# Optimization experiments

Hardware: AMD Instinct MI355X
Metric: run time of the kernel (lower is better)

The kernel has to match this reference:

```python
import jax, jax.numpy as jnp
import numpy as np

N_NODES = 100000
N_EDGES = 1600000
N_GRAPHS = 256
IN_F = 64   # global_features (GNN input dim)
OUT_F = 64  # node_features (GNN output dim)


def setup_inputs() -> dict:
    key = jax.random.key(0)
    ks = jax.random.split(key, 8)
    x = jax.random.normal(ks[0], (N_NODES, IN_F), dtype=jnp.float32)
    edge_index = jax.random.randint(ks[1], (2, N_EDGES), 0, N_NODES, dtype=jnp.int64)
    batch = jnp.sort(jax.random.randint(ks[2], (N_NODES,), 0, N_GRAPHS, dtype=jnp.int64))
    # GNNLayer linear: in=global_features, out=node_features
    W_gnn = jax.random.normal(ks[3], (IN_F, OUT_F), dtype=jnp.float32) / np.sqrt(IN_F)
    b_gnn = jnp.zeros((OUT_F,), dtype=jnp.float32)
    # global_attention: Linear(node_features, 1)
    W_att = jax.random.normal(ks[4], (OUT_F, 1), dtype=jnp.float32) / np.sqrt(OUT_F)
    b_att = jnp.zeros((1,), dtype=jnp.float32)
    return {"x": x, "edge_index": edge_index, "batch": batch,
            "W_gnn": W_gnn, "b_gnn": b_gnn, "W_att": W_att, "b_att": b_att}


def reference(x, edge_index, batch, W_gnn, b_gnn, W_att, b_att):
    src, dst = edge_index[0], edge_index[1]
    # --- GNN message passing layer: aggregate neighbor features, transform ---
    agg = jax.ops.segment_sum(x[src], dst, num_segments=N_NODES)  # [N, IN_F]
    h = jax.nn.relu((x + agg) @ W_gnn + b_gnn)                    # [N, OUT_F]
    # --- attention scores + scatter softmax over batch segments ---
    scores = (h @ W_att + b_att)[:, 0]                            # [N]
    seg_max = jax.ops.segment_max(scores, batch, num_segments=N_GRAPHS)
    e = jnp.exp(scores - seg_max[batch])
    denom = jax.ops.segment_sum(e, batch, num_segments=N_GRAPHS)
    w = e / denom[batch]                                          # [N]
    # --- weighted scatter-add pooling ---
    out = jax.ops.segment_sum(w[:, None] * h, batch, num_segments=N_GRAPHS)
    return out  # [N_GRAPHS, OUT_F]
```

## Files before the change

kernel.cpp:

```cpp
#include <hip/hip_runtime.h>

#define N_NODES  100000
#define N_EDGES  1600000
#define N_GRAPHS 256
#define F        64

#define CHUNK    8192
#define NCHUNK   196
#define GBN      128
#define NB2      782
#define EDGE_CAP 2560

#define CAST_ELEMS   (N_NODES * F / 4)
#define CAST_BLOCKS  ((CAST_ELEMS + 1023) / 1024)
#define CPF_BLOCKS   (NB2 + CAST_BLOCKS)

__device__ __forceinline__ unsigned short f2bf(float f) {
    unsigned int u = __float_as_uint(f);
    u += 0x7FFFu + ((u >> 16) & 1u);
    return (unsigned short)(u >> 16);
}

__global__ __launch_bounds__(1024) void prep_kernel(
        const int* __restrict__ src, const int* __restrict__ dst,
        unsigned int* __restrict__ pairs, int* __restrict__ cstartT) {
    __shared__ int hist[NB2];
    __shared__ int cur[NB2];
    __shared__ int wsum[16];
    __shared__ unsigned int stage[CHUNK];
    int tid  = threadIdx.x;
    int c    = blockIdx.x;
    int base = c * CHUNK;
    int m    = min(CHUNK, N_EDGES - base);
    int lane = tid & 63;
    int w    = tid >> 6;

    for (int k = tid; k < NB2; k += 1024) hist[k] = 0;
    __syncthreads();
    for (int e = tid; e < m; e += 1024)
        atomicAdd(&hist[dst[base + e] >> 7], 1);
    __syncthreads();

    int v = (tid < NB2) ? hist[tid] : 0;
    #pragma unroll
    for (int o = 1; o < 64; o <<= 1) {
        int u = __shfl_up(v, o, 64);
        if (lane >= o) v += u;
    }
    if (lane == 63) wsum[w] = v;
    __syncthreads();
    if (tid < 16) {
        int s = wsum[tid];
        #pragma unroll
        for (int o = 1; o < 16; o <<= 1) {
            int u = __shfl_up(s, o, 64);
            if (tid >= o) s += u;
        }
        wsum[tid] = s;
    }
    __syncthreads();
    if (w > 0) v += wsum[w - 1];

    if (tid < NB2) {
        int excl = v - hist[tid];
        cur[tid] = excl;
        cstartT[tid * NCHUNK + c] = base + excl;
    }
    if (tid == 0) cstartT[NB2 * NCHUNK + c] = base + m;
    __syncthreads();
    for (int e = tid; e < m; e += 1024) {
        int d = dst[base + e];
        int slot = atomicAdd(&cur[d >> 7], 1);
        stage[slot] = ((unsigned)(d & (GBN - 1)) << 17) | (unsigned)src[base + e];
    }
    __syncthreads();
    for (int e = tid; e < m; e += 1024)
        pairs[base + e] = stage[e];
}

__global__ __launch_bounds__(1024) void compact_cast_kernel(
        const unsigned int* __restrict__ pairs,
        const int* __restrict__ cstartT,
        int* __restrict__ eidx,
        int* __restrict__ nbeg,
        int* __restrict__ nend,
        const float* __restrict__ x,
        unsigned short* __restrict__ xh,
        float* __restrict__ out, float* __restrict__ denom) {
    int tid = threadIdx.x;
    int b   = blockIdx.x;

    if (b >= NB2) {
        int ci = b - NB2;
        if (ci == 0) {
            for (int i = tid; i < N_GRAPHS * F; i += 1024) out[i] = 0.f;
            if (tid < N_GRAPHS) denom[tid] = 0.f;
        }
        int i = ci * 1024 + tid;
        if (i < CAST_ELEMS) {
            float4 v = ((const float4*)x)[i];
            ushort4 o;
            o.x = f2bf(v.x); o.y = f2bf(v.y); o.z = f2bf(v.z); o.w = f2bf(v.w);
            ((ushort4*)xh)[i] = o;
        }
        return;
    }

    __shared__ int rstart[NCHUNK];
    __shared__ int roff[NCHUNK + 1];
    __shared__ int wsum[16];
    __shared__ unsigned int epairs[EDGE_CAP];
    __shared__ int ncnt[GBN];
    __shared__ int ncur[GBN];

    int wave  = tid >> 6;
    int lane  = tid & 63;
    int node0 = b * GBN;
    int nn    = min(GBN, N_NODES - node0);
    int gbase = b * EDGE_CAP;

    int myrc = 0;
    if (tid < NCHUNK) {
        int a = cstartT[b * NCHUNK + tid];
        int n = cstartT[(b + 1) * NCHUNK + tid];
        rstart[tid] = a;
        myrc = n - a;
    }
    __syncthreads();

    {
        int v = myrc;
        #pragma unroll
        for (int o = 1; o < 64; o <<= 1) {
            int u = __shfl_up(v, o, 64);
            if (lane >= o) v += u;
        }
        if (lane == 63) wsum[wave] = v;
        __syncthreads();
        if (tid < 16) {
            int s = wsum[tid];
            #pragma unroll
            for (int o = 1; o < 16; o <<= 1) {
                int u = __shfl_up(s, o, 64);
                if (tid >= o) s += u;
            }
            wsum[tid] = s;
        }
        __syncthreads();
        if (wave > 0) v += wsum[wave - 1];
        if (tid < NCHUNK) roff[tid] = v - myrc;
        if (tid == NCHUNK - 1) roff[NCHUNK] = v;
    }
    __syncthreads();
    int E = roff[NCHUNK];

    for (int e = tid; e < E; e += 1024) {
        int lo = 0, hi = NCHUNK - 1;
        while (lo < hi) {
            int mid = (lo + hi + 1) >> 1;
            if (roff[mid] <= e) lo = mid; else hi = mid - 1;
        }
        epairs[e] = pairs[rstart[lo] + (e - roff[lo])];
    }
    __syncthreads();

    if (tid < GBN) ncnt[tid] = 0;
    __syncthreads();
    for (int e = tid; e < E; e += 1024)
        atomicAdd(&ncnt[epairs[e] >> 17], 1);
    __syncthreads();
    {
        int mycnt = (tid < GBN) ? ncnt[tid] : 0;
        int v = mycnt;
        #pragma unroll
        for (int o = 1; o < 64; o <<= 1) {
            int u = __shfl_up(v, o, 64);
            if (lane >= o) v += u;
        }
        if (lane == 63) wsum[wave] = v;
        __syncthreads();
        if (tid < 2) {
            int s = wsum[tid];
            int u = __shfl_up(s, 1, 64);
            if (tid >= 1) s += u;
            wsum[tid] = s;
        }
        __syncthreads();
        if (wave == 1) v += wsum[0];
        if (tid < GBN) {
            int excl = v - mycnt;
            ncur[tid] = excl;
            if (tid < nn) {
                nbeg[node0 + tid] = gbase + excl;
                nend[node0 + tid] = gbase + excl + mycnt;
            }
        }
    }
    __syncthreads();
    for (int e = tid; e < E; e += 1024) {
        unsigned int p = epairs[e];
        int slot = atomicAdd(&ncur[p >> 17], 1);
        eidx[gbase + slot] = (int)(p & 0x1FFFFu);
    }
}

#define NODES_PER_WAVE 25
#define GT_NWAVES  (N_NODES / NODES_PER_WAVE)
#define GT_BLOCKS  (GT_NWAVES / 4)

__device__ __forceinline__ float bfl(unsigned int u) { return __uint_as_float(u << 16); }
__device__ __forceinline__ float bfh(unsigned int u) { return __uint_as_float(u & 0xFFFF0000u); }

__global__ __launch_bounds__(256) void gather_pool_kernel(
        const unsigned short* __restrict__ xh,
        const int*   __restrict__ nbeg,
        const int*   __restrict__ nend,
        const int*   __restrict__ eidx,
        const int*   __restrict__ batch,
        const float* __restrict__ Wg,
        const float* __restrict__ bg,
        const float* __restrict__ Wa,
        const float* __restrict__ ba,
        float*       __restrict__ out_acc,
        float*       __restrict__ denom) {
    int tid  = threadIdx.x;
    int lane = tid & 63;
    int grp  = lane >> 3;
    int c    = lane & 7;
    int waveId = blockIdx.x * 4 + (tid >> 6);

    int n0   = waveId * NODES_PER_WAVE;
    int nEnd = n0 + NODES_PER_WAVE;

    float wcol[F];
    #pragma unroll
    for (int k = 0; k < F; ++k) wcol[k] = Wg[k * F + lane];
    float bgl = bg[lane];
    float wal = Wa[lane];
    float ba0 = ba[0];

    const uint4* xh4 = (const uint4*)xh;

    int   cur_g = batch[n0];
    float accw  = 0.f;
    float denw  = 0.f;

    int pb = nbeg[n0];
    int pe = nend[n0];
    int sl_cur = (pb + lane < pe) ? eidx[pb + lane] : 0;

    for (int n = n0; n < nEnd; ++n) {
        int start = pb, end = pe;
        int sl    = sl_cur;
        if (n + 1 < nEnd) {
            pb = nbeg[n + 1];
            pe = nend[n + 1];
            sl_cur = (pb + lane < pe) ? eidx[pb + lane] : 0;
        }

        float a0=0.f,a1=0.f,a2=0.f,a3=0.f,a4=0.f,a5=0.f,a6=0.f,a7=0.f;
        {
            int jmax = end - start; if (jmax > 64) jmax = 64;
            for (int j = 0; j < jmax; j += 8) {
                int el = j + grp;
                int s  = __shfl(sl, el, 64);
                if (el < jmax) {
                    uint4 v = xh4[s * 8 + c];
                    a0 += bfl(v.x); a1 += bfh(v.x);
                    a2 += bfl(v.y); a3 += bfh(v.y);
                    a4 += bfl(v.z); a5 += bfh(v.z);
                    a6 += bfl(v.w); a7 += bfh(v.w);
                }
            }
        }
        for (int base = start + 64; base < end; base += 64) {
            int jmax = end - base; if (jmax > 64) jmax = 64;
            int sl2 = (base + lane < end) ? eidx[base + lane] : 0;
            for (int j = 0; j < jmax; j += 8) {
                int el = j + grp;
                int s  = __shfl(sl2, el, 64);
                if (el < jmax) {
                    uint4 v = xh4[s * 8 + c];
                    a0 += bfl(v.x); a1 += bfh(v.x);
                    a2 += bfl(v.y); a3 += bfh(v.y);
                    a4 += bfl(v.z); a5 += bfh(v.z);
                    a6 += bfl(v.w); a7 += bfh(v.w);
                }
            }
        }
        #pragma unroll
        for (int o = 8; o <= 32; o <<= 1) {
            a0 += __shfl_xor(a0, o, 64); a1 += __shfl_xor(a1, o, 64);
            a2 += __shfl_xor(a2, o, 64); a3 += __shfl_xor(a3, o, 64);
            a4 += __shfl_xor(a4, o, 64); a5 += __shfl_xor(a5, o, 64);
            a6 += __shfl_xor(a6, o, 64); a7 += __shfl_xor(a7, o, 64);
        }
        {
            uint4 v = xh4[n * 8 + c];
            a0 += bfl(v.x); a1 += bfh(v.x);
            a2 += bfl(v.y); a3 += bfh(v.y);
            a4 += bfl(v.z); a5 += bfh(v.z);
            a6 += bfl(v.w); a7 += bfh(v.w);
        }

        float re[8] = {a0,a1,a2,a3,a4,a5,a6,a7};
        float q0=0.f,q1=0.f,q2=0.f,q3=0.f,q4=0.f,q5=0.f,q6=0.f,q7=0.f;
        #pragma unroll
        for (int k = 0; k < F; k += 8) {
            int ln = k >> 3;
            q0 += __int_as_float(__builtin_amdgcn_readlane(__float_as_int(re[0]), ln)) * wcol[k + 0];
            q1 += __int_as_float(__builtin_amdgcn_readlane(__float_as_int(re[1]), ln)) * wcol[k + 1];
            q2 += __int_as_float(__builtin_amdgcn_readlane(__float_as_int(re[2]), ln)) * wcol[k + 2];
            q3 += __int_as_float(__builtin_amdgcn_readlane(__float_as_int(re[3]), ln)) * wcol[k + 3];
            q4 += __int_as_float(__builtin_amdgcn_readlane(__float_as_int(re[4]), ln)) * wcol[k + 4];
            q5 += __int_as_float(__builtin_amdgcn_readlane(__float_as_int(re[5]), ln)) * wcol[k + 5];
            q6 += __int_as_float(__builtin_amdgcn_readlane(__float_as_int(re[6]), ln)) * wcol[k + 6];
            q7 += __int_as_float(__builtin_amdgcn_readlane(__float_as_int(re[7]), ln)) * wcol[k + 7];
        }
        float hv = ((q0 + q1) + (q2 + q3)) + ((q4 + q5) + (q6 + q7)) + bgl;
        hv = hv > 0.f ? hv : 0.f;

        float p = hv * wal;
        #pragma unroll
        for (int o = 32; o > 0; o >>= 1)
            p += __shfl_down(p, o, 64);
        float s = __int_as_float(__builtin_amdgcn_readlane(__float_as_int(p), 0)) + ba0;
        float e = __expf(s);

        int g = batch[n];
        if (g != cur_g) {
            atomicAdd(&out_acc[cur_g * F + lane], accw);
            if (lane == 0) atomicAdd(&denom[cur_g], denw);
            accw = 0.f; denw = 0.f; cur_g = g;
        }
        accw += e * hv;
        denw += e;
    }
    atomicAdd(&out_acc[cur_g * F + lane], accw);
    if (lane == 0) atomicAdd(&denom[cur_g], denw);
}

__global__ __launch_bounds__(256) void finalize_kernel(
        float* __restrict__ out, const float* __restrict__ denom) {
    int i = blockIdx.x * 256 + threadIdx.x;
    if (i >= N_GRAPHS * F) return;
    float d = denom[i >> 6];
    out[i] = (d > 0.f) ? out[i] / d : 0.f;
}

extern "C" void kernel_launch(void* const* d_in, const int* in_sizes, int n_in,
                              void* d_out, int out_size, void* d_ws, size_t ws_size,
                              hipStream_t stream) {
    const float* x     = (const float*)d_in[0];
    const int*   ei    = (const int*)d_in[1];
    const int*   batch = (const int*)d_in[2];
    const float* Wg    = (const float*)d_in[3];
    const float* bg    = (const float*)d_in[4];
    const float* Wa    = (const float*)d_in[5];
    const float* ba    = (const float*)d_in[6];
    float* out = (float*)d_out;

    const int* src = ei;
    const int* dst = ei + N_EDGES;

    char* ws = (char*)d_ws;
    unsigned short* xh      = (unsigned short*)(ws);
    unsigned int*   pairs   = (unsigned int*)(ws + 12800000);
    int*            cstartT = (int*)(ws + 19200000);
    int*            eidx    = (int*)(ws + 19814144);
    int*            nbeg    = (int*)(ws + 27821824);
    int*            nend    = (int*)(ws + 28221824);
    float*          denom   = (float*)(ws + 28621824);

    prep_kernel        <<<NCHUNK, 1024, 0, stream>>>(src, dst, pairs, cstartT);
    compact_cast_kernel<<<CPF_BLOCKS, 1024, 0, stream>>>(
        pairs, cstartT, eidx, nbeg, nend, x, xh, out, denom);
    gather_pool_kernel <<<GT_BLOCKS, 256, 0, stream>>>(
        xh, nbeg, nend, eidx, batch, Wg, bg, Wa, ba, out, denom);
    finalize_kernel    <<<(N_GRAPHS * F + 255) / 256, 256, 0, stream>>>(out, denom);
}
```

Before: 183.7 us.

## Replace two-level bucketed CSR build with global atomic histogram and scatter

The chunked two-pass bucket sort (prep and compact) that built a per-node edge list is replaced by four simple kernels. They zero a per-node count, build a global atomic histogram over dst, give each wavefront a contiguous range through a global atomic allocator, and scatter src indices with per-node atomic cursors. This drops the shared-memory staging and binary searches, but it relies on heavy global atomics to random addresses, and the edge order and node ranges become nondeterministic and non-monotonic. It also adds kernel launches.

Result: slower. 366.6 us (+99.6%).

```diff
diff --git a/kernel.cpp b/kernel.cpp
--- a/kernel.cpp
+++ b/kernel.cpp
@@ -5,15 +5,8 @@
 #define N_GRAPHS 256
 #define F        64
 
-#define CHUNK    8192
-#define NCHUNK   196
-#define GBN      128
-#define NB2      782
-#define EDGE_CAP 2560
-
-#define CAST_ELEMS   (N_NODES * F / 4)
-#define CAST_BLOCKS  ((CAST_ELEMS + 1023) / 1024)
-#define CPF_BLOCKS   (NB2 + CAST_BLOCKS)
+#define CAST_ELEMS (N_NODES * F / 4)
+
 
 __device__ __forceinline__ unsigned short f2bf(float f) {
     unsigned int u = __float_as_uint(f);
@@ -21,186 +14,65 @@
     return (unsigned short)(u >> 16);
 }
 
-__global__ __launch_bounds__(1024) void prep_kernel(
-        const int* __restrict__ src, const int* __restrict__ dst,
-        unsigned int* __restrict__ pairs, int* __restrict__ cstartT) {
-    __shared__ int hist[NB2];
-    __shared__ int cur[NB2];
-    __shared__ int wsum[16];
-    __shared__ unsigned int stage[CHUNK];
-    int tid  = threadIdx.x;
-    int c    = blockIdx.x;
-    int base = c * CHUNK;
-    int m    = min(CHUNK, N_EDGES - base);
-    int lane = tid & 63;
-    int w    = tid >> 6;
-
-    for (int k = tid; k < NB2; k += 1024) hist[k] = 0;
-    __syncthreads();
-    for (int e = tid; e < m; e += 1024)
-        atomicAdd(&hist[dst[base + e] >> 7], 1);
-    __syncthreads();
-
-    int v = (tid < NB2) ? hist[tid] : 0;
+__global__ __launch_bounds__(256) void init_cast_kernel(
+        const float* __restrict__ x, unsigned short* __restrict__ xh,
+        int* __restrict__ cnt, float* __restrict__ out,
+        float* __restrict__ denom, unsigned int* __restrict__ allocp) {
+    int gtid   = blockIdx.x * 256 + threadIdx.x;
+    int stride = gridDim.x * 256;
+    for (int i = gtid; i < CAST_ELEMS; i += stride) {
+        float4 v = ((const float4*)x)[i];
+        ushort4 o;
+        o.x = f2bf(v.x); o.y = f2bf(v.y); o.z = f2bf(v.z); o.w = f2bf(v.w);
+        ((ushort4*)xh)[i] = o;
+    }
+    for (int i = gtid; i < N_NODES; i += stride) cnt[i] = 0;
+    if (gtid < N_GRAPHS * F) out[gtid] = 0.f;
+    if (gtid < N_GRAPHS) denom[gtid] = 0.f;
+    if (gtid == 0) *allocp = 0u;
+}
+
+__global__ __launch_bounds__(256) void hist_kernel(
+        const int* __restrict__ dst, int* __restrict__ cnt) {
+    int gtid   = blockIdx.x * 256 + threadIdx.x;
+    int stride = gridDim.x * 256;
+    for (int e = gtid; e < N_EDGES; e += stride)
+        atomicAdd(&cnt[dst[e]], 1);
+}
+
+__global__ __launch_bounds__(256) void alloc_kernel(
+        const int* __restrict__ cnt,
+        int* __restrict__ nbeg, int* __restrict__ nend, int* __restrict__ cur,
+        unsigned int* __restrict__ allocp) {
+    int i    = blockIdx.x * 256 + threadIdx.x;
+    int lane = threadIdx.x & 63;
+    int c = (i < N_NODES) ? cnt[i] : 0;
+    int v = c;
     #pragma unroll
     for (int o = 1; o < 64; o <<= 1) {
         int u = __shfl_up(v, o, 64);
         if (lane >= o) v += u;
     }
-    if (lane == 63) wsum[w] = v;
-    __syncthreads();
-    if (tid < 16) {
-        int s = wsum[tid];
-        #pragma unroll
-        for (int o = 1; o < 16; o <<= 1) {
-            int u = __shfl_up(s, o, 64);
-            if (tid >= o) s += u;
-        }
-        wsum[tid] = s;
-    }
-    __syncthreads();
-    if (w > 0) v += wsum[w - 1];
-
-    if (tid < NB2) {
-        int excl = v - hist[tid];
-        cur[tid] = excl;
-        cstartT[tid * NCHUNK + c] = base + excl;
-    }
-    if (tid == 0) cstartT[NB2 * NCHUNK + c] = base + m;
-    __syncthreads();
-    for (int e = tid; e < m; e += 1024) {
-        int d = dst[base + e];
-        int slot = atomicAdd(&cur[d >> 7], 1);
-        stage[slot] = ((unsigned)(d & (GBN - 1)) << 17) | (unsigned)src[base + e];
-    }
-    __syncthreads();
-    for (int e = tid; e < m; e += 1024)
-        pairs[base + e] = stage[e];
-}
-
-__global__ __launch_bounds__(1024) void compact_cast_kernel(
-        const unsigned int* __restrict__ pairs,
-        const int* __restrict__ cstartT,
-        int* __restrict__ eidx,
-        int* __restrict__ nbeg,
-        int* __restrict__ nend,
-        const float* __restrict__ x,
-        unsigned short* __restrict__ xh,
-        float* __restrict__ out, float* __restrict__ denom) {
-    int tid = threadIdx.x;
-    int b   = blockIdx.x;
-
-    if (b >= NB2) {
-        int ci = b - NB2;
-        if (ci == 0) {
-            for (int i = tid; i < N_GRAPHS * F; i += 1024) out[i] = 0.f;
-            if (tid < N_GRAPHS) denom[tid] = 0.f;
-        }
-        int i = ci * 1024 + tid;
-        if (i < CAST_ELEMS) {
-            float4 v = ((const float4*)x)[i];
-            ushort4 o;
-            o.x = f2bf(v.x); o.y = f2bf(v.y); o.z = f2bf(v.z); o.w = f2bf(v.w);
-            ((ushort4*)xh)[i] = o;
-        }
-        return;
-    }
-
-    __shared__ int rstart[NCHUNK];
-    __shared__ int roff[NCHUNK + 1];
-    __shared__ int wsum[16];
-    __shared__ unsigned int epairs[EDGE_CAP];
-    __shared__ int ncnt[GBN];
-    __shared__ int ncur[GBN];
-
-    int wave  = tid >> 6;
-    int lane  = tid & 63;
-    int node0 = b * GBN;
-    int nn    = min(GBN, N_NODES - node0);
-    int gbase = b * EDGE_CAP;
-
-    int myrc = 0;
-    if (tid < NCHUNK) {
-        int a = cstartT[b * NCHUNK + tid];
-        int n = cstartT[(b + 1) * NCHUNK + tid];
-        rstart[tid] = a;
-        myrc = n - a;
-    }
-    __syncthreads();
-
-    {
-        int v = myrc;
-        #pragma unroll
-        for (int o = 1; o < 64; o <<= 1) {
-            int u = __shfl_up(v, o, 64);
-            if (lane >= o) v += u;
-        }
-        if (lane == 63) wsum[wave] = v;
-        __syncthreads();
-        if (tid < 16) {
-            int s = wsum[tid];
-            #pragma unroll
-            for (int o = 1; o < 16; o <<= 1) {
-                int u = __shfl_up(s, o, 64);
-                if (tid >= o) s += u;
-            }
-            wsum[tid] = s;
-        }
-        __syncthreads();
-        if (wave > 0) v += wsum[wave - 1];
-        if (tid < NCHUNK) roff[tid] = v - myrc;
-        if (tid == NCHUNK - 1) roff[NCHUNK] = v;
-    }
-    __syncthreads();
-    int E = roff[NCHUNK];
-
-    for (int e = tid; e < E; e += 1024) {
-        int lo = 0, hi = NCHUNK - 1;
-        while (lo < hi) {
-            int mid = (lo + hi + 1) >> 1;
-            if (roff[mid] <= e) lo = mid; else hi = mid - 1;
-        }
-        epairs[e] = pairs[rstart[lo] + (e - roff[lo])];
-    }
-    __syncthreads();
-
-    if (tid < GBN) ncnt[tid] = 0;
-    __syncthreads();
-    for (int e = tid; e < E; e += 1024)
-        atomicAdd(&ncnt[epairs[e] >> 17], 1);
-    __syncthreads();
-    {
-        int mycnt = (tid < GBN) ? ncnt[tid] : 0;
-        int v = mycnt;
-        #pragma unroll
-        for (int o = 1; o < 64; o <<= 1) {
-            int u = __shfl_up(v, o, 64);
-            if (lane >= o) v += u;
-        }
-        if (lane == 63) wsum[wave] = v;
-        __syncthreads();
-        if (tid < 2) {
-            int s = wsum[tid];
-            int u = __shfl_up(s, 1, 64);
-            if (tid >= 1) s += u;
-            wsum[tid] = s;
-        }
-        __syncthreads();
-        if (wave == 1) v += wsum[0];
-        if (tid < GBN) {
-            int excl = v - mycnt;
-            ncur[tid] = excl;
-            if (tid < nn) {
-                nbeg[node0 + tid] = gbase + excl;
-                nend[node0 + tid] = gbase + excl + mycnt;
-            }
-        }
-    }
-    __syncthreads();
-    for (int e = tid; e < E; e += 1024) {
-        unsigned int p = epairs[e];
-        int slot = atomicAdd(&ncur[p >> 17], 1);
-        eidx[gbase + slot] = (int)(p & 0x1FFFFu);
+    int base = 0;
+    if (lane == 63) base = (int)atomicAdd(allocp, (unsigned int)v);
+    base = __shfl(base, 63, 64);
+    if (i < N_NODES) {
+        int b = base + v - c;
+        nbeg[i] = b;
+        nend[i] = b + c;
+        cur[i]  = b;
+    }
+}
+
+__global__ __launch_bounds__(256) void scatter_kernel(
+        const int* __restrict__ src, const int* __restrict__ dst,
+        int* __restrict__ cur, int* __restrict__ eidx) {
+    int gtid   = blockIdx.x * 256 + threadIdx.x;
+    int stride = gridDim.x * 256;
+    for (int e = gtid; e < N_EDGES; e += stride) {
+        int d = dst[e];
+        int slot = atomicAdd(&cur[d], 1);
+        eidx[slot] = src[e];
     }
 }
 
@@ -364,18 +236,20 @@
     const int* dst = ei + N_EDGES;
 
     char* ws = (char*)d_ws;
-    unsigned short* xh      = (unsigned short*)(ws);
-    unsigned int*   pairs   = (unsigned int*)(ws + 12800000);
-    int*            cstartT = (int*)(ws + 19200000);
-    int*            eidx    = (int*)(ws + 19814144);
-    int*            nbeg    = (int*)(ws + 27821824);
-    int*            nend    = (int*)(ws + 28221824);
-    float*          denom   = (float*)(ws + 28621824);
-
-    prep_kernel        <<<NCHUNK, 1024, 0, stream>>>(src, dst, pairs, cstartT);
-    compact_cast_kernel<<<CPF_BLOCKS, 1024, 0, stream>>>(
-        pairs, cstartT, eidx, nbeg, nend, x, xh, out, denom);
+    unsigned short* xh    = (unsigned short*)(ws);
+    int*            eidx  = (int*)(ws + 12800000);
+    int*            cnt   = (int*)(ws + 19200000);
+    int*            nbeg  = (int*)(ws + 19600000);
+    int*            nend  = (int*)(ws + 20000000);
+    int*            cur   = (int*)(ws + 20400000);
+    float*          denom = (float*)(ws + 20800000);
+    unsigned int*   allocp= (unsigned int*)(ws + 20801024);
+
+    init_cast_kernel<<<2048, 256, 0, stream>>>(x, xh, cnt, out, denom, allocp);
+    hist_kernel     <<<2048, 256, 0, stream>>>(dst, cnt);
+    alloc_kernel    <<<(N_NODES + 255) / 256, 256, 0, stream>>>(cnt, nbeg, nend, cur, allocp);
+    scatter_kernel  <<<2048, 256, 0, stream>>>(src, dst, cur, eidx);
     gather_pool_kernel <<<GT_BLOCKS, 256, 0, stream>>>(
         xh, nbeg, nend, eidx, batch, Wg, bg, Wa, ba, out, denom);
-    finalize_kernel    <<<(N_GRAPHS * F + 255) / 256, 256, 0, stream>>>(out, denom);
-}
+    finalize_kernel <<<(N_GRAPHS * F + 255) / 256, 256, 0, stream>>>(out, denom);
+}
```
